# Kernel optimization log

Hardware: AMD Instinct MI355X
Metric: run time of the kernel (lower is better)

Reference implementation:

```python
import jax, jax.numpy as jnp
import numpy as np

V, E, S, B, N, H = 32000, 1024, 1024, 4, 4, 16
DH = E // H
DFF = 4 * E
EPS = 1e-6


def _sinusoidal_pe(max_len, d):
    pos = np.arange(max_len)[:, None].astype(np.float32)
    div = np.power(10000.0, np.arange(0, d, 2).astype(np.float32) / d)
    pe = np.zeros((max_len, d), dtype=np.float32)
    pe[:, 0::2] = np.sin(pos / div)
    pe[:, 1::2] = np.cos(pos / div)
    return jnp.asarray(pe)


def layer_norm(x, g, b):
    mu = jnp.mean(x, axis=-1, keepdims=True)
    var = jnp.var(x, axis=-1, keepdims=True)
    return (x - mu) * jax.lax.rsqrt(var + EPS) * g + b


def setup_inputs() -> dict:
    key = jax.random.key(0)
    ks = iter(jax.random.split(key, 32))
    s = 0.02
    d = {}
    d['tokens'] = jax.random.randint(next(ks), (B, S), 0, V)
    d['emb'] = jax.random.normal(next(ks), (V, E), jnp.float32) * s
    d['pe'] = _sinusoidal_pe(S, E)
    # stacked per-layer params, leading dim N
    for name, shape in [('Wq', (N, E, E)), ('Wk', (N, E, E)), ('Wv', (N, E, E)), ('Wo', (N, E, E)),
                        ('W1', (N, E, DFF)), ('W2', (N, DFF, E))]:
        d[name] = jax.random.normal(next(ks), shape, jnp.float32) * s
    for name, shape in [('bq', (N, E)), ('bk', (N, E)), ('bv', (N, E)), ('bo', (N, E)),
                        ('b1', (N, DFF)), ('b2', (N, E))]:
        d[name] = jnp.zeros(shape, jnp.float32)
    d['ln1_g'] = jnp.ones((N, E)); d['ln1_b'] = jnp.zeros((N, E))
    d['ln2_g'] = jnp.ones((N, E)); d['ln2_b'] = jnp.zeros((N, E))
    d['enc_g'] = jnp.ones((E,)); d['enc_b'] = jnp.zeros((E,))
    d['fin_g'] = jnp.ones((E,)); d['fin_b'] = jnp.zeros((E,))
    d['Wout'] = jax.random.normal(next(ks), (E, V), jnp.float32) * s
    d['bout'] = jnp.zeros((V,), jnp.float32)
    return d


def _mha(x, Wq, bq, Wk, bk, Wv, bv, Wo, bo):
    b, s, _ = x.shape
    q = (x @ Wq + bq).reshape(b, s, H, DH)
    k = (x @ Wk + bk).reshape(b, s, H, DH)
    v = (x @ Wv + bv).reshape(b, s, H, DH)
    scores = jnp.einsum('bqhd,bkhd->bhqk', q, k) / jnp.sqrt(jnp.float32(DH))
    attn = jax.nn.softmax(scores, axis=-1)
    out = jnp.einsum('bhqk,bkhd->bqhd', attn, v).reshape(b, s, E)
    return out @ Wo + bo


def reference(tokens, emb, pe, Wq, bq, Wk, bk, Wv, bv, Wo, bo,
              W1, b1, W2, b2, ln1_g, ln1_b, ln2_g, ln2_b,
              enc_g, enc_b, fin_g, fin_b, Wout, bout):
    x = emb[tokens] + pe[None, :tokens.shape[1]]  # [B,S,E]; dropout = identity (eval)
    for i in range(N):
        # sublayer 0: x + LN(MHA(x))  (source's unusual residual order)
        a = _mha(x, Wq[i], bq[i], Wk[i], bk[i], Wv[i], bv[i], Wo[i], bo[i])
        x = x + layer_norm(a, ln1_g[i], ln1_b[i])
        # sublayer 1: x + LN(FF(x))
        f = jax.nn.relu(x @ W1[i] + b1[i]) @ W2[i] + b2[i]
        x = x + layer_norm(f, ln2_g[i], ln2_b[i])
    x = layer_norm(x, enc_g, enc_b)      # encoder final LN
    x = layer_norm(x, fin_g, fin_b)      # Transformer-level LN
    return x @ Wout + bout               # [B,S,V]
```

## Files before the change

kernel.cpp:

```cpp
#include <hip/hip_runtime.h>
#include <hip/hip_bf16.h>
#include <stdint.h>

#define EDIM 1024
#define DFFDIM 4096
#define NLAYER 4
#define BATCH 4
#define SEQ 1024
#define NHEAD 16
#define DHEAD 64
#define VOCAB 32000
#define MROWS (BATCH*SEQ)
#define QKVLD (3*EDIM)
#define EPSF 1e-6f
#define ALPHA 0.18033688011112043f

typedef float f32x4 __attribute__((ext_vector_type(4)));
typedef short s16x8 __attribute__((ext_vector_type(8)));
typedef __bf16 bf16x8 __attribute__((ext_vector_type(8)));

__device__ inline unsigned short f2bf(float f) {
  union { float f; uint32_t u; } v; v.f = f;
  uint32_t r = v.u + 0x7fffu + ((v.u >> 16) & 1u);
  return (unsigned short)(r >> 16);
}

__device__ __forceinline__ float fexp2(float x) {
  float r; asm("v_exp_f32 %0, %1" : "=v"(r) : "v"(x)); return r;
}
__device__ __forceinline__ uint32_t cvtpk(float lo, float hi) {
  uint32_t r; asm("v_cvt_pk_bf16_f32 %0, %1, %2" : "=v"(r) : "v"(lo), "v"(hi)); return r;
}

__device__ __forceinline__ void gload16(const void* g, void* l) {
  __builtin_amdgcn_global_load_lds(
      (const __attribute__((address_space(1))) void*)g,
      (__attribute__((address_space(3))) void*)l, 16, 0, 0);
}

__global__ __launch_bounds__(256) void embed_kernel(
    const int* __restrict__ tokens, const float* __restrict__ emb,
    const float* __restrict__ pe, float* __restrict__ x,
    unsigned short* __restrict__ xb) {
  const int row = blockIdx.x;
  const int s = row & (SEQ - 1);
  const int tok = tokens[row];
  const int c = threadIdx.x * 4;
  float4 ev = *(const float4*)(emb + (size_t)tok * EDIM + c);
  float4 pv = *(const float4*)(pe + (size_t)s * EDIM + c);
  float4 o;
  o.x = ev.x + pv.x; o.y = ev.y + pv.y; o.z = ev.z + pv.z; o.w = ev.w + pv.w;
  *(float4*)(x + (size_t)row * EDIM + c) = o;
  unsigned short* xr = xb + (size_t)row * EDIM + c;
  xr[0] = f2bf(o.x); xr[1] = f2bf(o.y); xr[2] = f2bf(o.z); xr[3] = f2bf(o.w);
}

__global__ __launch_bounds__(256) void transpose_w(
    const float* __restrict__ src, unsigned short* __restrict__ dst,
    int N, int K, float scale) {
  __shared__ float tl[64][65];
  const int t = threadIdx.x;
  const int k0 = blockIdx.x * 64, n0 = blockIdx.y * 64;
  const int c = (t & 15) * 4, r0 = t >> 4;
  #pragma unroll
  for (int i = 0; i < 4; ++i) {
    const int r = r0 + i * 16;
    float4 v = *(const float4*)(src + (size_t)(k0 + r) * N + n0 + c);
    tl[r][c] = v.x; tl[r][c + 1] = v.y; tl[r][c + 2] = v.z; tl[r][c + 3] = v.w;
  }
  __syncthreads();
  #pragma unroll
  for (int i = 0; i < 4; ++i) {
    const int n = r0 + i * 16;
    uint2 o;
    o.x = (uint32_t)f2bf(tl[c + 0][n] * scale) | ((uint32_t)f2bf(tl[c + 1][n] * scale) << 16);
    o.y = (uint32_t)f2bf(tl[c + 2][n] * scale) | ((uint32_t)f2bf(tl[c + 3][n] * scale) << 16);
    *(uint2*)(dst + (size_t)(n0 + n) * K + k0 + c) = o;
  }
}

__global__ __launch_bounds__(256) void pack_bias(
    const float* __restrict__ bq, const float* __restrict__ bk,
    const float* __restrict__ bv, float* __restrict__ dst) {
  const int idx = blockIdx.x * 256 + threadIdx.x;
  if (idx >= NLAYER * QKVLD) return;
  const int layer = idx / QKVLD, c = idx % QKVLD;
  float v;
  if (c < 1024)      v = bq[layer * 1024 + c] * ALPHA;
  else if (c < 2048) v = bk[layer * 1024 + c - 1024];
  else               v = bv[layer * 1024 + c - 2048];
  dst[idx] = v;
}

template<int BM, int OUT_BF16, int RELU>
__global__ __launch_bounds__(BM * 2, (BM == 256) ? 2 : 3) void gemm3(
    const unsigned short* __restrict__ A, const unsigned short* __restrict__ Bt,
    const float* __restrict__ bias, void* __restrict__ Cout,
    int Nld, int K, int NBLK, int G) {
  constexpr int BUFB = BM * 128;
  constexpr int ABYTES = BM * 64;
  constexpr int WN = (BM == 256) ? 4 : 2;
  constexpr int MF = BM / 32;
  __shared__ __attribute__((aligned(16))) char smb[3 * BUFB];
  const int t = threadIdx.x, lane = t & 63;
  const int wave = t >> 6;
  const int wr = wave / WN, wc = wave % WN;
  const int l15 = lane & 15, lg = lane >> 4;

  const int cpx = gridDim.x >> 3;
  const int bid = blockIdx.x;
  const int swz = (bid & 7) * cpx + (bid >> 3);
  const int sg = (gridDim.x / NBLK) * G;
  const int ns = swz / sg, rem = swz % sg;
  const int m0 = (rem / G) * BM;
  const int n0 = (ns * G + rem % G) * BM;

  f32x4 acc[MF][4];
  #pragma unroll
  for (int i = 0; i < MF; ++i)
    #pragma unroll
    for (int j = 0; j < 4; ++j)
      acc[i][j] = (f32x4){0.f, 0.f, 0.f, 0.f};

  const int srow = t >> 2;
  const int scol = (((t & 3) ^ ((t >> 3) & 3)) << 3);
  const unsigned short* agp = A  + (size_t)(m0 + srow) * K + scol;
  const unsigned short* bgp = Bt + (size_t)(n0 + srow) * K + scol;
  const size_t rhalf = (size_t)(BM / 2) * K;

  const int cxo = (lg * 16) ^ (((l15 >> 1) & 3) << 4);
  const int rdA = (wr * (BM / 2) + l15) * 64 + cxo;
  const int rdB = ABYTES + (wc * 64 + l15) * 64 + cxo;

  auto stage_tile = [&](int b, int kt) {
    const int k0 = kt * 32;
    char* d = smb + b * BUFB + t * 16;
    gload16(agp + k0, d);
    gload16(agp + rhalf + k0, d + BM * 32);
    gload16(bgp + k0, d + ABYTES);
    gload16(bgp + rhalf + k0, d + ABYTES + BM * 32);
  };

  const int NT = K / 32;
  stage_tile(0, 0);
  stage_tile(1, 1);
  asm volatile("s_waitcnt vmcnt(4)" ::: "memory");
  __builtin_amdgcn_s_barrier();
  __builtin_amdgcn_sched_barrier(0);

  int bufc = 0, bufn = 2;
  for (int tt = 0; tt < NT; ++tt) {
    if (tt + 2 < NT) stage_tile(bufn, tt + 2);

    const char* ab = smb + bufc * BUFB;
    bf16x8 af[MF], bf[4];
    #pragma unroll
    for (int mf = 0; mf < MF; ++mf)
      af[mf] = *(const bf16x8*)(ab + rdA + mf * 1024);
    #pragma unroll
    for (int nf = 0; nf < 4; ++nf)
      bf[nf] = *(const bf16x8*)(ab + rdB + nf * 1024);

    __builtin_amdgcn_s_setprio(1);
    #pragma unroll
    for (int mf = 0; mf < MF; ++mf)
      #pragma unroll
      for (int nf = 0; nf < 4; ++nf)
        acc[mf][nf] = __builtin_amdgcn_mfma_f32_16x16x32_bf16(af[mf], bf[nf], acc[mf][nf], 0, 0, 0);
    __builtin_amdgcn_s_setprio(0);

    if (tt + 2 < NT)      asm volatile("s_waitcnt vmcnt(4)" ::: "memory");
    else if (tt + 1 < NT) asm volatile("s_waitcnt vmcnt(0)" ::: "memory");
    __builtin_amdgcn_sched_barrier(0);
    __builtin_amdgcn_s_barrier();
    __builtin_amdgcn_sched_barrier(0);

    bufc = (bufc == 2) ? 0 : bufc + 1;
    bufn = (bufn == 2) ? 0 : bufn + 1;
  }

  #pragma unroll
  for (int mf = 0; mf < MF; ++mf) {
    #pragma unroll
    for (int nf = 0; nf < 4; ++nf) {
      const int col = n0 + wc * 64 + nf * 16 + l15;
      const float bv = bias[col];
      #pragma unroll
      for (int r = 0; r < 4; ++r) {
        const int row = m0 + wr * (BM / 2) + mf * 16 + lg * 4 + r;
        float val = acc[mf][nf][r] + bv;
        if (RELU) val = fmaxf(val, 0.f);
        if (OUT_BF16)
          ((unsigned short*)Cout)[(size_t)row * Nld + col] = f2bf(val);
        else
          ((float*)Cout)[(size_t)row * Nld + col] = val;
      }
    }
  }
}

__global__ __launch_bounds__(256) void attn_kernel(
    const unsigned short* __restrict__ qkv, unsigned short* __restrict__ ctx) {
  const int b = blockIdx.z, h = blockIdx.y;
  const int t = threadIdx.x, wave = t >> 6, lane = t & 63;
  const int l15 = lane & 15, lg = lane >> 4;
  const int qrow0 = blockIdx.x * 64 + wave * 16;
  const unsigned short* qbs = qkv + (size_t)b * SEQ * QKVLD + h * DHEAD;
  const unsigned short* kbs = qbs + EDIM;
  const unsigned short* vbs = qbs + 2 * EDIM;
  __shared__ unsigned short Ksm[64][72];
  __shared__ unsigned short VTs[64 * 64];

  const unsigned short* qp = qbs + (size_t)(qrow0 + l15) * QKVLD + lg * 8;
  bf16x8 a0 = *(const bf16x8*)qp;
  bf16x8 a1 = *(const bf16x8*)(qp + 32);

  f32x4 o[4];
  #pragma unroll
  for (int dg = 0; dg < 4; ++dg) o[dg] = (f32x4){0.f, 0.f, 0.f, 0.f};
  float m = -1e30f, ls = 0.f;

  const int sr = t >> 2;
  const int sc = (t & 3) * 16;
  const int posw = (((sr >> 4) & 1) << 5) | (((sr & 15) >> 2) << 3) | (((sr >> 5) & 1) << 2) | (sr & 3);
  const unsigned short* kgp = kbs + (size_t)sr * QKVLD + sc;
  const unsigned short* vgp = vbs + (size_t)sr * QKVLD + sc;
  const size_t tilestep = (size_t)64 * QKVLD;

  s16x8 kr0 = *(const s16x8*)kgp, kr1 = *(const s16x8*)(kgp + 8);
  s16x8 vr0 = *(const s16x8*)vgp, vr1 = *(const s16x8*)(vgp + 8);

  const int NT = SEQ / 64;
  for (int j = 0; j < NT; ++j) {
    *(s16x8*)&Ksm[sr][sc] = kr0;
    *(s16x8*)&Ksm[sr][sc + 8] = kr1;
    #pragma unroll
    for (int c = 0; c < 2; ++c) {
      s16x8 vv = c ? vr1 : vr0;
      #pragma unroll
      for (int e = 0; e < 8; ++e) {
        const int d = sc + c * 8 + e;
        const int byteo = d * 128 + ((posw * 2) ^ ((d & 7) << 4));
        *(unsigned short*)((char*)VTs + byteo) = (unsigned short)vv[e];
      }
    }
    __syncthreads();

    f32x4 s[4];
    __builtin_amdgcn_s_setprio(1);
    #pragma unroll
    for (int g = 0; g < 4; ++g) {
      bf16x8 k0 = *(const bf16x8*)&Ksm[g * 16 + l15][lg * 8];
      bf16x8 k1 = *(const bf16x8*)&Ksm[g * 16 + l15][32 + lg * 8];
      f32x4 z = {0, 0, 0, 0};
      z = __builtin_amdgcn_mfma_f32_16x16x32_bf16(k0, a0, z, 0, 0, 0);
      s[g] = __builtin_amdgcn_mfma_f32_16x16x32_bf16(k1, a1, z, 0, 0, 0);
    }
    __builtin_amdgcn_s_setprio(0);

    if (j + 1 < NT) {
      const unsigned short* kn = kgp + (size_t)(j + 1) * tilestep;
      const unsigned short* vn = vgp + (size_t)(j + 1) * tilestep;
      kr0 = *(const s16x8*)kn; kr1 = *(const s16x8*)(kn + 8);
      vr0 = *(const s16x8*)vn; vr1 = *(const s16x8*)(vn + 8);
    }

    float mx = s[0][0];
    #pragma unroll
    for (int g = 0; g < 4; ++g)
      #pragma unroll
      for (int r = 0; r < 4; ++r) mx = fmaxf(mx, s[g][r]);
    mx = fmaxf(mx, __shfl_xor(mx, 16));
    mx = fmaxf(mx, __shfl_xor(mx, 32));

    if (__any(mx > m + 8.f)) {
      const float mn = fmaxf(m, mx);
      const float scl = fexp2(m - mn);
      m = mn;
      ls *= scl;
      #pragma unroll
      for (int dg = 0; dg < 4; ++dg)
        #pragma unroll
        for (int r = 0; r < 4; ++r) o[dg][r] *= scl;
    }
    #pragma unroll
    for (int g = 0; g < 4; ++g)
      #pragma unroll
      for (int r = 0; r < 4; ++r) s[g][r] = fexp2(s[g][r] - m);

    float rs = 0.f;
    #pragma unroll
    for (int g = 0; g < 4; ++g)
      rs += (s[g][0] + s[g][1]) + (s[g][2] + s[g][3]);
    rs += __shfl_xor(rs, 16);
    rs += __shfl_xor(rs, 32);
    ls += rs;

    union { uint32_t u[4]; bf16x8 v; } pb0, pb1;
    pb0.u[0] = cvtpk(s[0][0], s[0][1]); pb0.u[1] = cvtpk(s[0][2], s[0][3]);
    pb0.u[2] = cvtpk(s[2][0], s[2][1]); pb0.u[3] = cvtpk(s[2][2], s[2][3]);
    pb1.u[0] = cvtpk(s[1][0], s[1][1]); pb1.u[1] = cvtpk(s[1][2], s[1][3]);
    pb1.u[2] = cvtpk(s[3][0], s[3][1]); pb1.u[3] = cvtpk(s[3][2], s[3][3]);

    auto vld = [&](int dg, int c) {
      const int byteo = (dg * 16 + l15) * 128 + ((c * 64 + lg * 16) ^ ((l15 & 7) << 4));
      return *(const bf16x8*)((const char*)VTs + byteo);
    };
    __builtin_amdgcn_s_setprio(1);
    #pragma unroll
    for (int dg = 0; dg < 4; ++dg)
      o[dg] = __builtin_amdgcn_mfma_f32_16x16x32_bf16(vld(dg, 0), pb0.v, o[dg], 0, 0, 0);
    #pragma unroll
    for (int dg = 0; dg < 4; ++dg)
      o[dg] = __builtin_amdgcn_mfma_f32_16x16x32_bf16(vld(dg, 1), pb1.v, o[dg], 0, 0, 0);
    __builtin_amdgcn_s_setprio(0);
    __syncthreads();
  }

  unsigned short* cp = ctx + (size_t)b * SEQ * EDIM + h * DHEAD + (size_t)(qrow0 + l15) * EDIM;
  const float inv = 1.f / ls;
  #pragma unroll
  for (int dg = 0; dg < 4; ++dg) {
    uint2 w;
    w.x = cvtpk(o[dg][0] * inv, o[dg][1] * inv);
    w.y = cvtpk(o[dg][2] * inv, o[dg][3] * inv);
    *(uint2*)(cp + dg * 16 + lg * 4) = w;
  }
}

__global__ __launch_bounds__(256) void ln_add_kernel(
    const float* __restrict__ a, const float* __restrict__ g, const float* __restrict__ bb,
    float* __restrict__ x, unsigned short* __restrict__ xb) {
  const int row = blockIdx.x, t = threadIdx.x;
  const float* ar = a + (size_t)row * EDIM;
  float4 av = *(const float4*)(ar + t * 4);
  float s = av.x + av.y + av.z + av.w;
  float qq = av.x * av.x + av.y * av.y + av.z * av.z + av.w * av.w;
  #pragma unroll
  for (int off = 1; off < 64; off <<= 1) { s += __shfl_xor(s, off); qq += __shfl_xor(qq, off); }
  __shared__ float red[8];
  const int wv = t >> 6;
  if ((t & 63) == 0) { red[wv] = s; red[4 + wv] = qq; }
  __syncthreads();
  s = red[0] + red[1] + red[2] + red[3];
  qq = red[4] + red[5] + red[6] + red[7];
  const float mean = s * (1.f / EDIM);
  const float rstd = rsqrtf(qq * (1.f / EDIM) - mean * mean + EPSF);
  float4 gv = *(const float4*)(g + t * 4);
  float4 bv = *(const float4*)(bb + t * 4);
  float* xr = x + (size_t)row * EDIM;
  float4 xv = *(float4*)(xr + t * 4);
  float4 o;
  o.x = xv.x + (av.x - mean) * rstd * gv.x + bv.x;
  o.y = xv.y + (av.y - mean) * rstd * gv.y + bv.y;
  o.z = xv.z + (av.z - mean) * rstd * gv.z + bv.z;
  o.w = xv.w + (av.w - mean) * rstd * gv.w + bv.w;
  *(float4*)(xr + t * 4) = o;
  unsigned short* xbr = xb + (size_t)row * EDIM + t * 4;
  xbr[0] = f2bf(o.x); xbr[1] = f2bf(o.y); xbr[2] = f2bf(o.z); xbr[3] = f2bf(o.w);
}

__global__ __launch_bounds__(256) void final_ln_kernel(
    const float* __restrict__ x, const float* __restrict__ g1, const float* __restrict__ b1,
    const float* __restrict__ g2, const float* __restrict__ b2,
    unsigned short* __restrict__ xb) {
  const int row = blockIdx.x, t = threadIdx.x;
  __shared__ float red[8];
  const int wv = t >> 6;
  const float* xr = x + (size_t)row * EDIM;
  float4 v = *(const float4*)(xr + t * 4);

  float s = v.x + v.y + v.z + v.w;
  float qq = v.x * v.x + v.y * v.y + v.z * v.z + v.w * v.w;
  #pragma unroll
  for (int off = 1; off < 64; off <<= 1) { s += __shfl_xor(s, off); qq += __shfl_xor(qq, off); }
  if ((t & 63) == 0) { red[wv] = s; red[4 + wv] = qq; }
  __syncthreads();
  s = red[0] + red[1] + red[2] + red[3];
  qq = red[4] + red[5] + red[6] + red[7];
  __syncthreads();
  float mean = s * (1.f / EDIM);
  float rstd = rsqrtf(qq * (1.f / EDIM) - mean * mean + EPSF);
  float4 g1v = *(const float4*)(g1 + t * 4);
  float4 b1v = *(const float4*)(b1 + t * 4);
  float4 tv;
  tv.x = (v.x - mean) * rstd * g1v.x + b1v.x;
  tv.y = (v.y - mean) * rstd * g1v.y + b1v.y;
  tv.z = (v.z - mean) * rstd * g1v.z + b1v.z;
  tv.w = (v.w - mean) * rstd * g1v.w + b1v.w;

  s = tv.x + tv.y + tv.z + tv.w;
  qq = tv.x * tv.x + tv.y * tv.y + tv.z * tv.z + tv.w * tv.w;
  #pragma unroll
  for (int off = 1; off < 64; off <<= 1) { s += __shfl_xor(s, off); qq += __shfl_xor(qq, off); }
  if ((t & 63) == 0) { red[wv] = s; red[4 + wv] = qq; }
  __syncthreads();
  s = red[0] + red[1] + red[2] + red[3];
  qq = red[4] + red[5] + red[6] + red[7];
  mean = s * (1.f / EDIM);
  rstd = rsqrtf(qq * (1.f / EDIM) - mean * mean + EPSF);
  float4 g2v = *(const float4*)(g2 + t * 4);
  float4 b2v = *(const float4*)(b2 + t * 4);
  unsigned short* o = xb + (size_t)row * EDIM + t * 4;
  o[0] = f2bf((tv.x - mean) * rstd * g2v.x + b2v.x);
  o[1] = f2bf((tv.y - mean) * rstd * g2v.y + b2v.y);
  o[2] = f2bf((tv.z - mean) * rstd * g2v.z + b2v.z);
  o[3] = f2bf((tv.w - mean) * rstd * g2v.w + b2v.w);
}

extern "C" void kernel_launch(void* const* d_in, const int* in_sizes, int n_in,
                              void* d_out, int out_size, void* d_ws, size_t ws_size,
                              hipStream_t stream) {
  const int*   tokens = (const int*)d_in[0];
  const float* emb    = (const float*)d_in[1];
  const float* pe     = (const float*)d_in[2];
  const float* Wq     = (const float*)d_in[3];
  const float* Wk     = (const float*)d_in[4];
  const float* Wv     = (const float*)d_in[5];
  const float* Wo     = (const float*)d_in[6];
  const float* W1     = (const float*)d_in[7];
  const float* W2     = (const float*)d_in[8];
  const float* bq     = (const float*)d_in[9];
  const float* bk     = (const float*)d_in[10];
  const float* bv     = (const float*)d_in[11];
  const float* bo     = (const float*)d_in[12];
  const float* b1     = (const float*)d_in[13];
  const float* b2     = (const float*)d_in[14];
  const float* ln1_g  = (const float*)d_in[15];
  const float* ln1_b  = (const float*)d_in[16];
  const float* ln2_g  = (const float*)d_in[17];
  const float* ln2_b  = (const float*)d_in[18];
  const float* enc_g  = (const float*)d_in[19];
  const float* enc_b  = (const float*)d_in[20];
  const float* fin_g  = (const float*)d_in[21];
  const float* fin_b  = (const float*)d_in[22];
  const float* Wout   = (const float*)d_in[23];
  const float* bout   = (const float*)d_in[24];
  float* out = (float*)d_out;

  uint8_t* p = (uint8_t*)d_ws;
  auto alloc = [&](size_t bytes) {
    void* r = (void*)p;
    p += (bytes + 255) & ~(size_t)255;
    return r;
  };
  float*          x     = (float*)alloc((size_t)MROWS * EDIM * 4);
  unsigned short* xb    = (unsigned short*)alloc((size_t)MROWS * EDIM * 2);
  float*          tbuf  = (float*)alloc((size_t)MROWS * EDIM * 4);
  unsigned short* qkv   = (unsigned short*)alloc((size_t)MROWS * QKVLD * 2);
  unsigned short* ctx   = (unsigned short*)alloc((size_t)MROWS * EDIM * 2);
  unsigned short* wlt   = (unsigned short*)alloc((size_t)NLAYER * 12 * 1024 * 1024 * 2);
  unsigned short* woutt = (unsigned short*)alloc((size_t)VOCAB * EDIM * 2);
  float*          bqkv  = (float*)alloc((size_t)NLAYER * QKVLD * 4);
  unsigned short* ff1   = qkv;
  if ((size_t)(p - (uint8_t*)d_ws) > ws_size) return;

  const dim3 blk(256);
  const dim3 blk512(512);
  const size_t LW = (size_t)12 * 1024 * 1024;
  const size_t M1 = 1024 * 1024;

  for (int i = 0; i < NLAYER; ++i) {
    unsigned short* lb = wlt + (size_t)i * LW;
    transpose_w<<<dim3(16, 16),  blk, 0, stream>>>(Wq + (size_t)i * M1, lb,          1024, 1024, ALPHA);
    transpose_w<<<dim3(16, 16),  blk, 0, stream>>>(Wk + (size_t)i * M1, lb + M1,     1024, 1024, 1.0f);
    transpose_w<<<dim3(16, 16),  blk, 0, stream>>>(Wv + (size_t)i * M1, lb + 2 * M1, 1024, 1024, 1.0f);
    transpose_w<<<dim3(16, 16),  blk, 0, stream>>>(Wo + (size_t)i * M1, lb + 3 * M1, 1024, 1024, 1.0f);
    transpose_w<<<dim3(16, 64),  blk, 0, stream>>>(W1 + (size_t)i * 4 * M1, lb + 4 * M1, 4096, 1024, 1.0f);
    transpose_w<<<dim3(64, 16),  blk, 0, stream>>>(W2 + (size_t)i * 4 * M1, lb + 8 * M1, 1024, 4096, 1.0f);
  }
  transpose_w<<<dim3(16, 500), blk, 0, stream>>>(Wout, woutt, VOCAB, 1024, 1.0f);
  pack_bias<<<(NLAYER * QKVLD + 255) / 256, blk, 0, stream>>>(bq, bk, bv, bqkv);

  embed_kernel<<<MROWS, blk, 0, stream>>>(tokens, emb, pe, x, xb);

  const int MB2 = MROWS / 256;
  const int MB1 = MROWS / 128;
  for (int i = 0; i < NLAYER; ++i) {
    unsigned short* lb = wlt + (size_t)i * LW;
    gemm3<256, 1, 0><<<MB2 * (QKVLD / 256), blk512, 0, stream>>>(
        xb, lb, bqkv + (size_t)i * QKVLD, qkv, QKVLD, EDIM, QKVLD / 256, 4);
    attn_kernel<<<dim3(SEQ / 64, NHEAD, BATCH), blk, 0, stream>>>(qkv, ctx);
    gemm3<128, 0, 0><<<MB1 * (EDIM / 128), blk, 0, stream>>>(
        ctx, lb + 3 * M1, bo + i * EDIM, tbuf, EDIM, EDIM, EDIM / 128, 4);
    ln_add_kernel<<<MROWS, blk, 0, stream>>>(tbuf, ln1_g + i * EDIM, ln1_b + i * EDIM, x, xb);
    gemm3<256, 1, 1><<<MB2 * (DFFDIM / 256), blk512, 0, stream>>>(
        xb, lb + 4 * M1, b1 + i * DFFDIM, ff1, DFFDIM, EDIM, DFFDIM / 256, 4);
    gemm3<128, 0, 0><<<MB1 * (EDIM / 128), blk, 0, stream>>>(
        ff1, lb + 8 * M1, b2 + i * EDIM, tbuf, EDIM, DFFDIM, EDIM / 128, 2);
    ln_add_kernel<<<MROWS, blk, 0, stream>>>(tbuf, ln2_g + i * EDIM, ln2_b + i * EDIM, x, xb);
  }

  final_ln_kernel<<<MROWS, blk, 0, stream>>>(x, enc_g, enc_b, fin_g, fin_b, xb);
  gemm3<256, 0, 0><<<MB2 * (VOCAB / 256), blk512, 0, stream>>>(
      xb, woutt, bout, out, VOCAB, EDIM, VOCAB / 256, 5);
}
```

Measured before the change: 1.342 ms.

## Add split-K for N=1024 GEMMs, smaller QKV/FF1 tiles, batch weight transposes

The Wo and W2 projections (N=1024) now split K in two across a second grid dimension. Each half writes its partial sum to a separate fp32 buffer, and the following LayerNorm-add kernel sums the two buffers before normalising. The QKV and FF1 GEMMs drop from 256-row to 128-row tiles with a larger swizzle group, and the per-layer weight transposes are merged into one z-batched launch per matrix. The intent is more blocks for the narrow GEMMs on the many CUs and fewer launches. The cost is an extra 16MB fp32 partial buffer write and read per projection, plus a fallback path if workspace is short.

```diff
diff --git a/kernel.cpp b/kernel.cpp
--- a/kernel.cpp
+++ b/kernel.cpp
@@ -56,8 +56,10 @@
 }
 
 __global__ __launch_bounds__(256) void transpose_w(
-    const float* __restrict__ src, unsigned short* __restrict__ dst,
-    int N, int K, float scale) {
+    const float* __restrict__ src0, unsigned short* __restrict__ dst0,
+    int N, int K, float scale, size_t srcStride, size_t dstStride) {
+  const float* src = src0 + (size_t)blockIdx.z * srcStride;
+  unsigned short* dst = dst0 + (size_t)blockIdx.z * dstStride;
   __shared__ float tl[64][65];
   const int t = threadIdx.x;
   const int k0 = blockIdx.x * 64, n0 = blockIdx.y * 64;
@@ -92,11 +94,11 @@
   dst[idx] = v;
 }
 
-template<int BM, int OUT_BF16, int RELU>
+template<int BM, int OUT_BF16, int RELU, int SPLITK>
 __global__ __launch_bounds__(BM * 2, (BM == 256) ? 2 : 3) void gemm3(
     const unsigned short* __restrict__ A, const unsigned short* __restrict__ Bt,
-    const float* __restrict__ bias, void* __restrict__ Cout,
-    int Nld, int K, int NBLK, int G) {
+    const float* __restrict__ bias, void* __restrict__ Cout, void* __restrict__ C2,
+    int Nld, int KLEN, int KLD, int NBLK, int G) {
   constexpr int BUFB = BM * 128;
   constexpr int ABYTES = BM * 64;
   constexpr int WN = (BM == 256) ? 4 : 2;
@@ -114,6 +116,7 @@
   const int ns = swz / sg, rem = swz % sg;
   const int m0 = (rem / G) * BM;
   const int n0 = (ns * G + rem % G) * BM;
+  const int koff = SPLITK ? blockIdx.y * KLEN : 0;
 
   f32x4 acc[MF][4];
   #pragma unroll
@@ -124,9 +127,9 @@
 
   const int srow = t >> 2;
   const int scol = (((t & 3) ^ ((t >> 3) & 3)) << 3);
-  const unsigned short* agp = A  + (size_t)(m0 + srow) * K + scol;
-  const unsigned short* bgp = Bt + (size_t)(n0 + srow) * K + scol;
-  const size_t rhalf = (size_t)(BM / 2) * K;
+  const unsigned short* agp = A  + (size_t)(m0 + srow) * KLD + scol + koff;
+  const unsigned short* bgp = Bt + (size_t)(n0 + srow) * KLD + scol + koff;
+  const size_t rhalf = (size_t)(BM / 2) * KLD;
 
   const int cxo = (lg * 16) ^ (((l15 >> 1) & 3) << 4);
   const int rdA = (wr * (BM / 2) + l15) * 64 + cxo;
@@ -141,7 +144,7 @@
     gload16(bgp + rhalf + k0, d + ABYTES + BM * 32);
   };
 
-  const int NT = K / 32;
+  const int NT = KLEN / 32;
   stage_tile(0, 0);
   stage_tile(1, 1);
   asm volatile("s_waitcnt vmcnt(4)" ::: "memory");
@@ -179,21 +182,22 @@
     bufn = (bufn == 2) ? 0 : bufn + 1;
   }
 
+  void* Cw = (SPLITK && blockIdx.y) ? C2 : Cout;
   #pragma unroll
   for (int mf = 0; mf < MF; ++mf) {
     #pragma unroll
     for (int nf = 0; nf < 4; ++nf) {
       const int col = n0 + wc * 64 + nf * 16 + l15;
-      const float bv = bias[col];
+      const float bv = (SPLITK && blockIdx.y) ? 0.f : bias[col];
       #pragma unroll
       for (int r = 0; r < 4; ++r) {
         const int row = m0 + wr * (BM / 2) + mf * 16 + lg * 4 + r;
         float val = acc[mf][nf][r] + bv;
         if (RELU) val = fmaxf(val, 0.f);
         if (OUT_BF16)
-          ((unsigned short*)Cout)[(size_t)row * Nld + col] = f2bf(val);
+          ((unsigned short*)Cw)[(size_t)row * Nld + col] = f2bf(val);
         else
-          ((float*)Cout)[(size_t)row * Nld + col] = val;
+          ((float*)Cw)[(size_t)row * Nld + col] = val;
       }
     }
   }
@@ -328,12 +332,17 @@
   }
 }
 
+template<int TWO>
 __global__ __launch_bounds__(256) void ln_add_kernel(
-    const float* __restrict__ a, const float* __restrict__ g, const float* __restrict__ bb,
+    const float* __restrict__ a, const float* __restrict__ a2,
+    const float* __restrict__ g, const float* __restrict__ bb,
     float* __restrict__ x, unsigned short* __restrict__ xb) {
   const int row = blockIdx.x, t = threadIdx.x;
-  const float* ar = a + (size_t)row * EDIM;
-  float4 av = *(const float4*)(ar + t * 4);
+  float4 av = *(const float4*)(a + (size_t)row * EDIM + t * 4);
+  if (TWO) {
+    float4 a2v = *(const float4*)(a2 + (size_t)row * EDIM + t * 4);
+    av.x += a2v.x; av.y += a2v.y; av.z += a2v.z; av.w += a2v.w;
+  }
   float s = av.x + av.y + av.z + av.w;
   float qq = av.x * av.x + av.y * av.y + av.z * av.z + av.w * av.w;
   #pragma unroll
@@ -454,22 +463,21 @@
   float*          bqkv  = (float*)alloc((size_t)NLAYER * QKVLD * 4);
   unsigned short* ff1   = qkv;
   if ((size_t)(p - (uint8_t*)d_ws) > ws_size) return;
+  float* tbuf2 = (float*)alloc((size_t)MROWS * EDIM * 4);
+  const bool have2 = (size_t)(p - (uint8_t*)d_ws) <= ws_size;
 
   const dim3 blk(256);
   const dim3 blk512(512);
   const size_t LW = (size_t)12 * 1024 * 1024;
   const size_t M1 = 1024 * 1024;
 
-  for (int i = 0; i < NLAYER; ++i) {
-    unsigned short* lb = wlt + (size_t)i * LW;
-    transpose_w<<<dim3(16, 16),  blk, 0, stream>>>(Wq + (size_t)i * M1, lb,          1024, 1024, ALPHA);
-    transpose_w<<<dim3(16, 16),  blk, 0, stream>>>(Wk + (size_t)i * M1, lb + M1,     1024, 1024, 1.0f);
-    transpose_w<<<dim3(16, 16),  blk, 0, stream>>>(Wv + (size_t)i * M1, lb + 2 * M1, 1024, 1024, 1.0f);
-    transpose_w<<<dim3(16, 16),  blk, 0, stream>>>(Wo + (size_t)i * M1, lb + 3 * M1, 1024, 1024, 1.0f);
-    transpose_w<<<dim3(16, 64),  blk, 0, stream>>>(W1 + (size_t)i * 4 * M1, lb + 4 * M1, 4096, 1024, 1.0f);
-    transpose_w<<<dim3(64, 16),  blk, 0, stream>>>(W2 + (size_t)i * 4 * M1, lb + 8 * M1, 1024, 4096, 1.0f);
-  }
-  transpose_w<<<dim3(16, 500), blk, 0, stream>>>(Wout, woutt, VOCAB, 1024, 1.0f);
+  transpose_w<<<dim3(16, 16, NLAYER), blk, 0, stream>>>(Wq, wlt,          1024, 1024, ALPHA, M1, LW);
+  transpose_w<<<dim3(16, 16, NLAYER), blk, 0, stream>>>(Wk, wlt + M1,     1024, 1024, 1.0f,  M1, LW);
+  transpose_w<<<dim3(16, 16, NLAYER), blk, 0, stream>>>(Wv, wlt + 2 * M1, 1024, 1024, 1.0f,  M1, LW);
+  transpose_w<<<dim3(16, 16, NLAYER), blk, 0, stream>>>(Wo, wlt + 3 * M1, 1024, 1024, 1.0f,  M1, LW);
+  transpose_w<<<dim3(16, 64, NLAYER), blk, 0, stream>>>(W1, wlt + 4 * M1, 4096, 1024, 1.0f, 4 * M1, LW);
+  transpose_w<<<dim3(64, 16, NLAYER), blk, 0, stream>>>(W2, wlt + 8 * M1, 1024, 4096, 1.0f, 4 * M1, LW);
+  transpose_w<<<dim3(16, 500), blk, 0, stream>>>(Wout, woutt, VOCAB, 1024, 1.0f, 0, 0);
   pack_bias<<<(NLAYER * QKVLD + 255) / 256, blk, 0, stream>>>(bq, bk, bv, bqkv);
 
   embed_kernel<<<MROWS, blk, 0, stream>>>(tokens, emb, pe, x, xb);
@@ -478,20 +486,32 @@
   const int MB1 = MROWS / 128;
   for (int i = 0; i < NLAYER; ++i) {
     unsigned short* lb = wlt + (size_t)i * LW;
-    gemm3<256, 1, 0><<<MB2 * (QKVLD / 256), blk512, 0, stream>>>(
-        xb, lb, bqkv + (size_t)i * QKVLD, qkv, QKVLD, EDIM, QKVLD / 256, 4);
+    gemm3<128, 1, 0, 0><<<MB1 * (QKVLD / 128), blk, 0, stream>>>(
+        xb, lb, bqkv + (size_t)i * QKVLD, qkv, nullptr, QKVLD, EDIM, EDIM, QKVLD / 128, 8);
     attn_kernel<<<dim3(SEQ / 64, NHEAD, BATCH), blk, 0, stream>>>(qkv, ctx);
-    gemm3<128, 0, 0><<<MB1 * (EDIM / 128), blk, 0, stream>>>(
-        ctx, lb + 3 * M1, bo + i * EDIM, tbuf, EDIM, EDIM, EDIM / 128, 4);
-    ln_add_kernel<<<MROWS, blk, 0, stream>>>(tbuf, ln1_g + i * EDIM, ln1_b + i * EDIM, x, xb);
-    gemm3<256, 1, 1><<<MB2 * (DFFDIM / 256), blk512, 0, stream>>>(
-        xb, lb + 4 * M1, b1 + i * DFFDIM, ff1, DFFDIM, EDIM, DFFDIM / 256, 4);
-    gemm3<128, 0, 0><<<MB1 * (EDIM / 128), blk, 0, stream>>>(
-        ff1, lb + 8 * M1, b2 + i * EDIM, tbuf, EDIM, DFFDIM, EDIM / 128, 2);
-    ln_add_kernel<<<MROWS, blk, 0, stream>>>(tbuf, ln2_g + i * EDIM, ln2_b + i * EDIM, x, xb);
+    if (have2) {
+      gemm3<128, 0, 0, 1><<<dim3(MB1 * (EDIM / 128), 2), blk, 0, stream>>>(
+          ctx, lb + 3 * M1, bo + i * EDIM, tbuf, tbuf2, EDIM, EDIM / 2, EDIM, EDIM / 128, 8);
+      ln_add_kernel<1><<<MROWS, blk, 0, stream>>>(tbuf, tbuf2, ln1_g + i * EDIM, ln1_b + i * EDIM, x, xb);
+    } else {
+      gemm3<128, 0, 0, 0><<<MB1 * (EDIM / 128), blk, 0, stream>>>(
+          ctx, lb + 3 * M1, bo + i * EDIM, tbuf, nullptr, EDIM, EDIM, EDIM, EDIM / 128, 8);
+      ln_add_kernel<0><<<MROWS, blk, 0, stream>>>(tbuf, nullptr, ln1_g + i * EDIM, ln1_b + i * EDIM, x, xb);
+    }
+    gemm3<128, 1, 1, 0><<<MB1 * (DFFDIM / 128), blk, 0, stream>>>(
+        xb, lb + 4 * M1, b1 + i * DFFDIM, ff1, nullptr, DFFDIM, EDIM, EDIM, DFFDIM / 128, 8);
+    if (have2) {
+      gemm3<128, 0, 0, 1><<<dim3(MB1 * (EDIM / 128), 2), blk, 0, stream>>>(
+          ff1, lb + 8 * M1, b2 + i * EDIM, tbuf, tbuf2, EDIM, DFFDIM / 2, DFFDIM, EDIM / 128, 8);
+      ln_add_kernel<1><<<MROWS, blk, 0, stream>>>(tbuf, tbuf2, ln2_g + i * EDIM, ln2_b + i * EDIM, x, xb);
+    } else {
+      gemm3<128, 0, 0, 0><<<MB1 * (EDIM / 128), blk, 0, stream>>>(
+          ff1, lb + 8 * M1, b2 + i * EDIM, tbuf, nullptr, EDIM, DFFDIM, DFFDIM, EDIM / 128, 8);
+      ln_add_kernel<0><<<MROWS, blk, 0, stream>>>(tbuf, nullptr, ln2_g + i * EDIM, ln2_b + i * EDIM, x, xb);
+    }
   }
 
   final_ln_kernel<<<MROWS, blk, 0, stream>>>(x, enc_g, enc_b, fin_g, fin_b, xb);
-  gemm3<256, 0, 0><<<MB2 * (VOCAB / 256), blk512, 0, stream>>>(
-      xb, woutt, bout, out, VOCAB, EDIM, VOCAB / 256, 5);
-}
+  gemm3<256, 0, 0, 0><<<MB2 * (VOCAB / 256), blk512, 0, stream>>>(
+      xb, woutt, bout, out, nullptr, VOCAB, EDIM, EDIM, VOCAB / 256, 5);
+}
```

Result: no change. 1.318 ms (-1.8%).
